# Kernel tuning notes

Hardware: AMD Instinct MI355X
Metric: run time of the kernel (lower is better)

The kernel has to match this reference:

```python
import jax, jax.numpy as jnp
import numpy as np

HEADS = 8
DIM_HEAD = 64
DIM = 512
HIDDEN = HEADS * DIM_HEAD  # 512


def setup_inputs() -> dict:
    key = jax.random.key(0)
    k1, k2, k3, k4 = jax.random.split(key, 4)
    b, m, n = 4, 8, 512
    x = jax.random.normal(k1, (b, m, n, DIM), dtype=jnp.float32)
    pos_bias = jax.random.normal(k2, (HEADS, n, 16, 16), dtype=jnp.float32)
    # torch nn.Linear(dim, 3*hidden) weight is [3*hidden, dim]; we store the
    # transposed matmul form [dim, 3*hidden] for y = x @ W.
    w_qkv = jax.random.normal(k3, (DIM, 3 * HIDDEN), dtype=jnp.float32) * (DIM ** -0.5)
    w_out = jax.random.normal(k4, (HIDDEN, DIM), dtype=jnp.float32) * (HIDDEN ** -0.5)
    return {"x": x, "pos_bias": pos_bias, "w_qkv": w_qkv, "w_out": w_out}


def reference(x, pos_bias, w_qkv, w_out):
    b, m, n, _ = x.shape
    h, d = HEADS, DIM_HEAD
    scale = d ** -0.5
    qkv = jnp.einsum('bmnc,ce->bmne', x, w_qkv)  # [b,m,n,3*hidden]
    q, k, v = jnp.split(qkv, 3, axis=-1)
    # 'b m n (h d) -> (b m) h n d'
    def to_heads(t):
        return t.reshape(b * m, n, h, d).transpose(0, 2, 1, 3)
    q, k, v = to_heads(q), to_heads(k), to_heads(v)
    q = q * scale
    sim = jnp.einsum('bhid,bhjd->bhij', q, k)  # [(b*m), h, n, n]
    # pos_bias [h, n, p, q] -> mean over last two dims -> [h, n] -> broadcast [1,h,n,1]
    pb = pos_bias.mean(axis=(-2, -1))[None, :, :, None]
    sim = sim + pb
    sim = sim - jax.lax.stop_gradient(jnp.max(sim, axis=-1, keepdims=True))
    attn = jax.nn.softmax(sim, axis=-1)
    out = jnp.einsum('bhij,bhjd->bhid', attn, v)  # [(b*m), h, n, d]
    # '(b m) h n d -> b m n (h d)'
    out = out.transpose(0, 2, 1, 3).reshape(b, m, n, h * d)
    return jnp.einsum('bmne,ec->bmnc', out, w_out)
```

## Files before the change

### kernel.cpp

```cpp
#include <hip/hip_runtime.h>
#include <stdint.h>


typedef __attribute__((ext_vector_type(8))) short bf16x8;
typedef __attribute__((ext_vector_type(4))) float f32x4;
typedef __attribute__((ext_vector_type(4))) unsigned short us4;
typedef __attribute__((ext_vector_type(4))) float float4v;

__device__ __forceinline__ unsigned short f2b(float f) {
  union { float f; uint32_t u; } x; x.f = f;
  uint32_t r = x.u + 0x7fffu + ((x.u >> 16) & 1u);
  return (unsigned short)(r >> 16);
}

__device__ __forceinline__ uint32_t cvtpk(float lo, float hi) {
  uint32_t r;
  asm("v_cvt_pk_bf16_f32 %0, %1, %2" : "=v"(r) : "v"(lo), "v"(hi));
  return r;
}

__device__ __forceinline__ f32x4 mfma16(bf16x8 a, bf16x8 b, f32x4 c) {
  return __builtin_amdgcn_mfma_f32_16x16x32_bf16(a, b, c, 0, 0, 0);
}

__device__ __forceinline__ void gload_lds16(const unsigned short* g, unsigned short* l) {
  __builtin_amdgcn_global_load_lds(
      (const __attribute__((address_space(1))) unsigned int*)g,
      (__attribute__((address_space(3))) unsigned int*)l, 16, 0, 0);
}

__global__ __launch_bounds__(256) void prep_kernel(
    const float* __restrict__ x, unsigned short* __restrict__ xb,
    const float* __restrict__ wq, unsigned short* __restrict__ wqbT,
    const float* __restrict__ wo, unsigned short* __restrict__ wobT) {
  const int bid = blockIdx.x;
  if (bid < 8192) {
    size_t i = ((size_t)bid * 256 + threadIdx.x) * 4;
    float4v v = *(const float4v*)(x + i);
    us4 o;
#pragma unroll
    for (int j = 0; j < 4; ++j) o[j] = f2b(v[j]);
    *(us4*)(xb + i) = o;
    return;
  }
  __shared__ float tile[64][65];
  const float* src;
  unsigned short* dst;
  int R, C, bx, by;
  float scl = 1.0f;
  if (bid < 8192 + 192) {
    int q = bid - 8192;
    src = wq; dst = wqbT; R = 512; C = 1536; bx = q % 24; by = q / 24;
    if (bx * 64 < 512) scl = 0.125f;
  } else {
    int q = bid - 8384;
    src = wo; dst = wobT; R = 512; C = 512; bx = q % 8; by = q / 8;
  }
  const int tc0 = bx * 64, tr0 = by * 64;
#pragma unroll
  for (int k2 = 0; k2 < 16; ++k2) {
    int idx = threadIdx.x + k2 * 256;
    int r = idx >> 6, c = idx & 63;
    tile[r][c] = src[(size_t)(tr0 + r) * C + tc0 + c];
  }
  __syncthreads();
#pragma unroll
  for (int k2 = 0; k2 < 16; ++k2) {
    int idx = threadIdx.x + k2 * 256;
    int c = idx >> 6, r = idx & 63;
    dst[(size_t)(tc0 + c) * R + tr0 + r] = f2b(tile[r][c] * scl);
  }
}

__device__ __forceinline__ void gemm_core(
    const unsigned short* __restrict__ A, const unsigned short* __restrict__ Bt,
    int r0, int c0, unsigned short* As, unsigned short* Bs,
    f32x4 (&acc)[4][4]) {
  const int tid = threadIdx.x;
  const int lane = tid & 63;
  const int wave = tid >> 6;
  const int wr = (wave >> 1) * 64;
  const int wc = (wave & 1) * 64;
  const int l15 = lane & 15;
  const int g = lane >> 4;
  const int rsw = (l15 >> 1) & 3;

#pragma unroll
  for (int m = 0; m < 4; ++m)
#pragma unroll
    for (int n = 0; n < 4; ++n) acc[m][n] = (f32x4){0.f, 0.f, 0.f, 0.f};

  auto stage_half = [&](int t) {
    const int off = ((t >> 1) & 1) * 8192 + (t & 1) * 4096;
    const int kt = t * 32;
#pragma unroll
    for (int i = 0; i < 2; ++i) {
      int chunk = tid + i * 256;
      int row = chunk >> 2;
      int cg = (chunk & 3) ^ ((row >> 1) & 3);
      gload_lds16(A + (size_t)(r0 + row) * 512 + kt + cg * 8, As + off + chunk * 8);
      gload_lds16(Bt + (size_t)(c0 + row) * 512 + kt + cg * 8, Bs + off + chunk * 8);
    }
  };

  stage_half(0);
  stage_half(1);
  stage_half(2);

#pragma unroll
  for (int t = 0; t < 16; ++t) {
    if (t <= 13)      asm volatile("s_waitcnt vmcnt(8)" ::: "memory");
    else if (t == 14) asm volatile("s_waitcnt vmcnt(4)" ::: "memory");
    else              asm volatile("s_waitcnt vmcnt(0)" ::: "memory");
    __builtin_amdgcn_s_barrier();
    if (t + 3 < 16) stage_half(t + 3);
    const int off = ((t >> 1) & 1) * 8192 + (t & 1) * 4096;
    const unsigned short* as = As + off;
    const unsigned short* bs = Bs + off;
    bf16x8 af[4], bfr[4];
#pragma unroll
    for (int m = 0; m < 4; ++m)
      af[m] = *(const bf16x8*)(as + ((wr + m * 16 + l15) * 4 + (g ^ rsw)) * 8);
#pragma unroll
    for (int n = 0; n < 4; ++n)
      bfr[n] = *(const bf16x8*)(bs + ((wc + n * 16 + l15) * 4 + (g ^ rsw)) * 8);
    __builtin_amdgcn_s_setprio(1);
#pragma unroll
    for (int m = 0; m < 4; ++m)
#pragma unroll
      for (int n = 0; n < 4; ++n) acc[m][n] = mfma16(af[m], bfr[n], acc[m][n]);
    __builtin_amdgcn_s_setprio(0);
  }
  __syncthreads();
}

__global__ __launch_bounds__(256) void gemm_qkv_kernel(
    const unsigned short* __restrict__ xb, const unsigned short* __restrict__ wqbT,
    unsigned short* __restrict__ qb, unsigned short* __restrict__ kb,
    unsigned short* __restrict__ vtb) {
  __shared__ unsigned short As[16384];
  __shared__ unsigned short Bs[16384];
  f32x4 acc[4][4];
  const int r0 = blockIdx.x * 128;
  const int c0 = blockIdx.y * 128;
  gemm_core(xb, wqbT, r0, c0, As, Bs, acc);

  const int tid = threadIdx.x, lane = tid & 63, wave = tid >> 6;
  const int wr = (wave >> 1) * 64, wc = (wave & 1) * 64;
  const int l15 = lane & 15, g = lane >> 4;
  const int part = c0 >> 9;

  if (part < 2) {
#pragma unroll
    for (int m = 0; m < 4; ++m) {
      int rbase = wr + m * 16 + 4 * g;
#pragma unroll
      for (int n = 0; n < 4; ++n) {
        int c = wc + n * 16 + l15;
        int c2 = c >> 3, ci = c & 7;
#pragma unroll
        for (int rr = 0; rr < 4; ++rr) {
          int r = rbase + rr;
          As[r * 128 + ((c2 ^ (r & 15)) << 3) + ci] = f2b(acc[m][n][rr]);
        }
      }
    }
    __syncthreads();
    unsigned short* dstb = (part == 0) ? qb : kb;
#pragma unroll
    for (int it = 0; it < 8; ++it) {
      int idx = tid + it * 256;
      int r = idx >> 4, c2 = idx & 15;
      bf16x8 v = *(const bf16x8*)(As + r * 128 + ((c2 ^ (r & 15)) << 3));
      int e = c0 + c2 * 8;
      int rem = e & 511, h = rem >> 6, d = rem & 63;
      int ig = r0 + r;
      int bh = (ig >> 9) * 8 + h, i = ig & 511;
      *(bf16x8*)(dstb + ((size_t)bh * 512 + i) * 64 + d) = v;
    }
  } else {
#pragma unroll
    for (int m = 0; m < 4; ++m) {
      int rbase = wr + m * 16 + 4 * g;
      int r2 = rbase >> 3, rhalf = rbase & 7;
#pragma unroll
      for (int n = 0; n < 4; ++n) {
        int c = wc + n * 16 + l15;
        us4 v;
#pragma unroll
        for (int rr = 0; rr < 4; ++rr) v[rr] = f2b(acc[m][n][rr]);
        *(us4*)(As + c * 128 + ((r2 ^ (c & 15)) << 3) + rhalf) = v;
      }
    }
    __syncthreads();
#pragma unroll
    for (int it = 0; it < 8; ++it) {
      int idx = tid + it * 256;
      int c = idx >> 4, r8 = idx & 15;
      bf16x8 v = *(const bf16x8*)(As + c * 128 + ((r8 ^ (c & 15)) << 3));
      int e = c0 + c;
      int rem = e & 511, h = rem >> 6, d = rem & 63;
      int ig0 = r0 + r8 * 8;
      int bh = (ig0 >> 9) * 8 + h, i = ig0 & 511;
      *(bf16x8*)(vtb + ((size_t)bh * 64 + d) * 512 + i) = v;
    }
  }
}

__global__ __launch_bounds__(256) void gemm_out_kernel(
    const unsigned short* __restrict__ ao, const unsigned short* __restrict__ wobT,
    float* __restrict__ out) {
  __shared__ unsigned short As[16384];
  __shared__ unsigned short Bs[16384];
  f32x4 acc[4][4];
  const int r0 = blockIdx.x * 128;
  const int c0 = blockIdx.y * 128;
  gemm_core(ao, wobT, r0, c0, As, Bs, acc);

  const int tid = threadIdx.x, lane = tid & 63, wave = tid >> 6;
  const int wr = (wave >> 1) * 64, wc = (wave & 1) * 64;
  const int l15 = lane & 15, g = lane >> 4;
#pragma unroll
  for (int m = 0; m < 4; ++m) {
    int i0g = r0 + wr + m * 16 + 4 * g;
#pragma unroll
    for (int n = 0; n < 4; ++n) {
      int e = c0 + wc + n * 16 + l15;
#pragma unroll
      for (int rr = 0; rr < 4; ++rr)
        out[(size_t)(i0g + rr) * 512 + e] = acc[m][n][rr];
    }
  }
}

__global__ __launch_bounds__(512, 6) void attn_kernel(
    const unsigned short* __restrict__ qb, const unsigned short* __restrict__ kb,
    const unsigned short* __restrict__ vtb, unsigned short* __restrict__ ao) {
  __shared__ unsigned short kbuf[2][4096];
  __shared__ unsigned short vbuf[2][4096];
  __shared__ unsigned short Ps[8][16][40];
  const int bh = blockIdx.x;
  const int qt = blockIdx.y;
  const int tid = threadIdx.x, lane = tid & 63, wave = tid >> 6;
  const int l15 = lane & 15, g = lane >> 4;
  const int qrow0 = qt * 128 + wave * 16;

  const unsigned short* Q = qb + ((size_t)bh * 512 + qrow0) * 64;
  const unsigned short* Kp = kb + (size_t)bh * 512 * 64;
  const unsigned short* Vt = vtb + (size_t)bh * 64 * 512;

  bf16x8 qf0 = *(const bf16x8*)(Q + l15 * 64 + g * 8);
  bf16x8 qf1 = *(const bf16x8*)(Q + l15 * 64 + 32 + g * 8);

  const int srow = tid >> 3;
  const int sck = (tid & 7) ^ (srow & 7);

  auto stage = [&](int t, int b) {
    gload_lds16(Kp + (size_t)(t * 64 + srow) * 64 + sck * 8, kbuf[b] + tid * 8);
    gload_lds16(Vt + (size_t)srow * 512 + t * 64 + sck * 8, vbuf[b] + tid * 8);
  };

  f32x4 oacc[4];
#pragma unroll
  for (int m = 0; m < 4; ++m) oacc[m] = (f32x4){0.f, 0.f, 0.f, 0.f};
  float srowsum[4] = {0.f, 0.f, 0.f, 0.f};

  stage(0, 0);
  asm volatile("s_waitcnt vmcnt(0)" ::: "memory");
  __builtin_amdgcn_s_barrier();

  int cur = 0;
#pragma unroll
  for (int t = 0; t < 8; ++t) {
    if (t < 7) stage(t + 1, cur ^ 1);

    const unsigned short* kb_ = kbuf[cur];
    f32x4 s[4];
    const int c0i = g ^ (l15 & 7);
    __builtin_amdgcn_s_setprio(1);
#pragma unroll
    for (int tt = 0; tt < 4; ++tt) {
      int row = tt * 16 + l15;
      bf16x8 b0 = *(const bf16x8*)(kb_ + (row * 8 + c0i) * 8);
      bf16x8 b1 = *(const bf16x8*)(kb_ + (row * 8 + (c0i ^ 4)) * 8);
      f32x4 c = (f32x4){0.f, 0.f, 0.f, 0.f};
      c = mfma16(qf0, b0, c);
      s[tt] = mfma16(qf1, b1, c);
    }
    __builtin_amdgcn_s_setprio(0);

#pragma unroll
    for (int tt = 0; tt < 4; ++tt)
#pragma unroll
      for (int rr = 0; rr < 4; ++rr) {
        float e = __expf(s[tt][rr]);
        s[tt][rr] = e;
        srowsum[rr] += e;
      }

    const unsigned short* vb_ = vbuf[cur];
#pragma unroll
    for (int cc = 0; cc < 2; ++cc) {
#pragma unroll
      for (int rr = 0; rr < 4; ++rr) {
        uint32_t pk = cvtpk(s[cc * 2][rr], s[cc * 2 + 1][rr]);
        Ps[wave][4 * g + rr][l15] = (unsigned short)pk;
        Ps[wave][4 * g + rr][16 + l15] = (unsigned short)(pk >> 16);
      }
      asm volatile("s_waitcnt lgkmcnt(0)" ::: "memory");
      bf16x8 pf = *(const bf16x8*)(&Ps[wave][l15][g * 8]);
      __builtin_amdgcn_s_setprio(1);
#pragma unroll
      for (int m = 0; m < 4; ++m) {
        int vr = m * 16 + l15;
        bf16x8 vf = *(const bf16x8*)(vb_ + (vr * 8 + ((cc * 4 + g) ^ (l15 & 7))) * 8);
        oacc[m] = mfma16(vf, pf, oacc[m]);
      }
      __builtin_amdgcn_s_setprio(0);
    }

    if (t < 7) {
      asm volatile("s_waitcnt vmcnt(0)" ::: "memory");
      __builtin_amdgcn_s_barrier();
      cur ^= 1;
    }
  }

#pragma unroll
  for (int rr = 0; rr < 4; ++rr)
#pragma unroll
    for (int o = 1; o < 16; o <<= 1) srowsum[rr] += __shfl_xor(srowsum[rr], o);
  int srcl = (l15 >> 2) * 16;
  float t0 = __shfl(srowsum[0], srcl), t1 = __shfl(srowsum[1], srcl);
  float t2 = __shfl(srowsum[2], srcl), t3 = __shfl(srowsum[3], srcl);
  int rq = l15 & 3;
  float sq = rq == 0 ? t0 : rq == 1 ? t1 : rq == 2 ? t2 : t3;
  float invq = 1.0f / sq;

  const int hh = bh & 7, bm = bh >> 3;
  unsigned short* aorow = ao + ((size_t)bm * 512 + qrow0 + l15) * 512 + hh * 64;
#pragma unroll
  for (int m = 0; m < 4; ++m) {
    union { us4 u; uint32_t w[2]; } uv;
    uv.w[0] = cvtpk(oacc[m][0] * invq, oacc[m][1] * invq);
    uv.w[1] = cvtpk(oacc[m][2] * invq, oacc[m][3] * invq);
    *(us4*)(aorow + m * 16 + 4 * g) = uv.u;
  }
}

extern "C" void kernel_launch(void* const* d_in, const int* in_sizes, int n_in,
                              void* d_out, int out_size, void* d_ws, size_t ws_size,
                              hipStream_t stream) {
  const float* x = (const float*)d_in[0];
  const float* w_qkv = (const float*)d_in[2];
  const float* w_out = (const float*)d_in[3];
  float* out = (float*)d_out;

  char* ws = (char*)d_ws;
  const size_t SZ_XB = 16384ull * 512 * 2;
  const size_t SZ_WQ = 1536ull * 512 * 2;
  const size_t SZ_WO = 512ull * 512 * 2;
  const size_t SZ_HB = 256ull * 512 * 64 * 2;
  unsigned short* xb = (unsigned short*)(ws);
  unsigned short* wqbT = (unsigned short*)(ws + SZ_XB);
  unsigned short* wobT = (unsigned short*)(ws + SZ_XB + SZ_WQ);
  unsigned short* qb = (unsigned short*)(ws + SZ_XB + SZ_WQ + SZ_WO);
  unsigned short* kb = (unsigned short*)(ws + SZ_XB + SZ_WQ + SZ_WO + SZ_HB);
  unsigned short* vtb = (unsigned short*)(ws + SZ_XB + SZ_WQ + SZ_WO + 2 * SZ_HB);
  unsigned short* ao = (unsigned short*)(ws + SZ_XB + SZ_WQ + SZ_WO + 3 * SZ_HB);

  prep_kernel<<<8448, 256, 0, stream>>>(x, xb, w_qkv, wqbT, w_out, wobT);
  gemm_qkv_kernel<<<dim3(128, 12), 256, 0, stream>>>(xb, wqbT, qb, kb, vtb);
  attn_kernel<<<dim3(256, 4), 512, 0, stream>>>(qb, kb, vtb, ao);
  gemm_out_kernel<<<dim3(128, 4), 256, 0, stream>>>(ao, wobT, out);
}
```

Baseline: 101.9 us.

## Switch GEMM staging from 4-deep ring to double buffer with smaller LDS

Replaces the four-slot LDS ring (three tiles in flight, partial vmcnt waits) in the shared GEMM core with a two-slot double buffer that prefetches one k-tile ahead and waits for all loads before each barrier. LDS per block shrinks from 64 KB to 32 KB by sharing one array for A and B tiles, which may allow more resident blocks per CU. The cost is less prefetch depth, so global-load latency is less hidden behind MFMA work within a block.

```diff
diff --git a/kernel.cpp b/kernel.cpp
--- a/kernel.cpp
+++ b/kernel.cpp
@@ -90,33 +90,29 @@
 #pragma unroll
     for (int n = 0; n < 4; ++n) acc[m][n] = (f32x4){0.f, 0.f, 0.f, 0.f};
 
-  auto stage_half = [&](int t) {
-    const int off = ((t >> 1) & 1) * 8192 + (t & 1) * 4096;
-    const int kt = t * 32;
+  auto stage = [&](int t, int b) {
 #pragma unroll
     for (int i = 0; i < 2; ++i) {
       int chunk = tid + i * 256;
       int row = chunk >> 2;
       int cg = (chunk & 3) ^ ((row >> 1) & 3);
-      gload_lds16(A + (size_t)(r0 + row) * 512 + kt + cg * 8, As + off + chunk * 8);
-      gload_lds16(Bt + (size_t)(c0 + row) * 512 + kt + cg * 8, Bs + off + chunk * 8);
+      gload_lds16(A + (size_t)(r0 + row) * 512 + t * 32 + cg * 8,
+                  As + b * 4096 + chunk * 8);
+      gload_lds16(Bt + (size_t)(c0 + row) * 512 + t * 32 + cg * 8,
+                  Bs + b * 4096 + chunk * 8);
     }
   };
 
-  stage_half(0);
-  stage_half(1);
-  stage_half(2);
-
+  stage(0, 0);
+  asm volatile("s_waitcnt vmcnt(0)" ::: "memory");
+  __builtin_amdgcn_s_barrier();
+
+  int cur = 0;
 #pragma unroll
   for (int t = 0; t < 16; ++t) {
-    if (t <= 13)      asm volatile("s_waitcnt vmcnt(8)" ::: "memory");
-    else if (t == 14) asm volatile("s_waitcnt vmcnt(4)" ::: "memory");
-    else              asm volatile("s_waitcnt vmcnt(0)" ::: "memory");
-    __builtin_amdgcn_s_barrier();
-    if (t + 3 < 16) stage_half(t + 3);
-    const int off = ((t >> 1) & 1) * 8192 + (t & 1) * 4096;
-    const unsigned short* as = As + off;
-    const unsigned short* bs = Bs + off;
+    if (t < 15) stage(t + 1, cur ^ 1);
+    const unsigned short* as = As + cur * 4096;
+    const unsigned short* bs = Bs + cur * 4096;
     bf16x8 af[4], bfr[4];
 #pragma unroll
     for (int m = 0; m < 4; ++m)
@@ -130,6 +126,11 @@
 #pragma unroll
       for (int n = 0; n < 4; ++n) acc[m][n] = mfma16(af[m], bfr[n], acc[m][n]);
     __builtin_amdgcn_s_setprio(0);
+    if (t < 15) {
+      asm volatile("s_waitcnt vmcnt(0)" ::: "memory");
+      __builtin_amdgcn_s_barrier();
+      cur ^= 1;
+    }
   }
   __syncthreads();
 }
@@ -138,12 +139,11 @@
     const unsigned short* __restrict__ xb, const unsigned short* __restrict__ wqbT,
     unsigned short* __restrict__ qb, unsigned short* __restrict__ kb,
     unsigned short* __restrict__ vtb) {
-  __shared__ unsigned short As[16384];
-  __shared__ unsigned short Bs[16384];
+  __shared__ unsigned short smem[16384];
   f32x4 acc[4][4];
   const int r0 = blockIdx.x * 128;
   const int c0 = blockIdx.y * 128;
-  gemm_core(xb, wqbT, r0, c0, As, Bs, acc);
+  gemm_core(xb, wqbT, r0, c0, smem, smem + 8192, acc);
 
   const int tid = threadIdx.x, lane = tid & 63, wave = tid >> 6;
   const int wr = (wave >> 1) * 64, wc = (wave & 1) * 64;
@@ -161,7 +161,7 @@
 #pragma unroll
         for (int rr = 0; rr < 4; ++rr) {
           int r = rbase + rr;
-          As[r * 128 + ((c2 ^ (r & 15)) << 3) + ci] = f2b(acc[m][n][rr]);
+          smem[r * 128 + ((c2 ^ (r & 15)) << 3) + ci] = f2b(acc[m][n][rr]);
         }
       }
     }
@@ -171,7 +171,7 @@
     for (int it = 0; it < 8; ++it) {
       int idx = tid + it * 256;
       int r = idx >> 4, c2 = idx & 15;
-      bf16x8 v = *(const bf16x8*)(As + r * 128 + ((c2 ^ (r & 15)) << 3));
+      bf16x8 v = *(const bf16x8*)(smem + r * 128 + ((c2 ^ (r & 15)) << 3));
       int e = c0 + c2 * 8;
       int rem = e & 511, h = rem >> 6, d = rem & 63;
       int ig = r0 + r;
@@ -189,7 +189,7 @@
         us4 v;
 #pragma unroll
         for (int rr = 0; rr < 4; ++rr) v[rr] = f2b(acc[m][n][rr]);
-        *(us4*)(As + c * 128 + ((r2 ^ (c & 15)) << 3) + rhalf) = v;
+        *(us4*)(smem + c * 128 + ((r2 ^ (c & 15)) << 3) + rhalf) = v;
       }
     }
     __syncthreads();
@@ -197,7 +197,7 @@
     for (int it = 0; it < 8; ++it) {
       int idx = tid + it * 256;
       int c = idx >> 4, r8 = idx & 15;
-      bf16x8 v = *(const bf16x8*)(As + c * 128 + ((r8 ^ (c & 15)) << 3));
+      bf16x8 v = *(const bf16x8*)(smem + c * 128 + ((r8 ^ (c & 15)) << 3));
       int e = c0 + c;
       int rem = e & 511, h = rem >> 6, d = rem & 63;
       int ig0 = r0 + r8 * 8;
@@ -210,12 +210,11 @@
 __global__ __launch_bounds__(256) void gemm_out_kernel(
     const unsigned short* __restrict__ ao, const unsigned short* __restrict__ wobT,
     float* __restrict__ out) {
-  __shared__ unsigned short As[16384];
-  __shared__ unsigned short Bs[16384];
+  __shared__ unsigned short smem[16384];
   f32x4 acc[4][4];
   const int r0 = blockIdx.x * 128;
   const int c0 = blockIdx.y * 128;
-  gemm_core(ao, wobT, r0, c0, As, Bs, acc);
+  gemm_core(ao, wobT, r0, c0, smem, smem + 8192, acc);
 
   const int tid = threadIdx.x, lane = tid & 63, wave = tid >> 6;
   const int wr = (wave >> 1) * 64, wc = (wave & 1) * 64;
```

After: 97.40 us. 4.4% less time.
